# Kernel optimization log

Measured on AMD Instinct MI355X. Metric: run time of the kernel, lower is better.

The kernel has to match this reference:

```python
import jax, jax.numpy as jnp
import numpy as np

DIM = 1024
NUM_HEADS = 16
DIM_HEAD = 64
FEATURE_DIM = 64
INNER = NUM_HEADS * DIM_HEAD
EPS = 1e-6


def setup_inputs() -> dict:
    key = jax.random.key(0)
    ks = jax.random.split(key, 7)
    x = jax.random.normal(ks[0], (4, 8192, DIM), dtype=jnp.float32)
    s = 1.0 / np.sqrt(DIM)
    Wq = jax.random.normal(ks[1], (DIM, INNER), dtype=jnp.float32) * s
    Wk = jax.random.normal(ks[2], (DIM, INNER), dtype=jnp.float32) * s
    Wv = jax.random.normal(ks[3], (DIM, INNER), dtype=jnp.float32) * s
    proj = jax.random.normal(ks[4], (DIM_HEAD, FEATURE_DIM), dtype=jnp.float32) / np.sqrt(FEATURE_DIM)
    Wo = jax.random.normal(ks[5], (INNER, DIM), dtype=jnp.float32) * (1.0 / np.sqrt(INNER))
    bo = jnp.zeros((DIM,), dtype=jnp.float32)
    return {"x": x, "Wq": Wq, "Wk": Wk, "Wv": Wv, "proj": proj, "Wo": Wo, "bo": bo}


def _feature_map(t, proj):
    # t: [b, h, n, d] -> relu(t @ proj) + eps : [b, h, n, f]
    return jax.nn.relu(jnp.einsum('bhnd,df->bhnf', t, proj)) + EPS


def reference(x, Wq, Wk, Wv, proj, Wo, bo):
    b, n, _ = x.shape
    def split_heads(t):
        return t.reshape(b, n, NUM_HEADS, DIM_HEAD).transpose(0, 2, 1, 3)  # [b,h,n,d]
    q = split_heads(x @ Wq)
    k = split_heads(x @ Wk)
    v = split_heads(x @ Wv)
    qf = _feature_map(q, proj)  # [b,h,n,f]
    kf = _feature_map(k, proj)  # [b,h,n,f]
    kv = jnp.einsum('bhnf,bhnd->bhfd', kf, v)          # [b,h,f,d]
    k_sum = kf.sum(axis=-2)                             # [b,h,f]
    num = jnp.einsum('bhnf,bhfd->bhnd', qf, kv)         # [b,h,n,d]
    den = jnp.einsum('bhnf,bhf->bhn', qf, k_sum) + EPS  # [b,h,n]
    out = num / den[..., None]
    out = out.transpose(0, 2, 1, 3).reshape(b, n, INNER)
    return out @ Wo + bo
```

## Files before the change

### kernel.cpp

```cpp
#include <hip/hip_runtime.h>

typedef unsigned short u16;
typedef unsigned int u32;
typedef __attribute__((ext_vector_type(4))) float f32x4;
typedef __attribute__((ext_vector_type(4))) u16 u16x4;
typedef __attribute__((ext_vector_type(8))) u16 u16x8;
typedef __attribute__((ext_vector_type(8))) __bf16 bf16x8;

#define FLA_EPS 1e-6f

__device__ __forceinline__ u16 f2b(float f) {
  union { float f; u32 u; } v; v.f = f;
  u32 r = v.u + 0x7FFFu + ((v.u >> 16) & 1u);
  return (u16)(r >> 16);
}
__device__ __forceinline__ float b2f(u16 h) {
  union { u32 u; float f; } v; v.u = ((u32)h) << 16; return v.f;
}
__device__ __forceinline__ float bsum8(bf16x8 v) {
  union { bf16x8 b; u16x8 u; } x; x.b = v;
  float s = 0.f;
#pragma unroll
  for (int e = 0; e < 8; ++e) s += b2f(x.u[e]);
  return s;
}
__device__ __forceinline__ void g2l16(const void* g, void* l) {
  __builtin_amdgcn_global_load_lds((__attribute__((address_space(1))) void*)g,
                                   (__attribute__((address_space(3))) void*)l,
                                   16, 0, 0);
}

__global__ void __launch_bounds__(256) cast_f32_bf16(const float* __restrict__ in,
                                                     u16* __restrict__ out) {
  size_t i = (size_t)blockIdx.x * 256 + threadIdx.x;
  const f32x4* p = (const f32x4*)in + i * 2;
  f32x4 a = p[0], b = p[1];
  u16x8 r;
  r[0] = f2b(a[0]); r[1] = f2b(a[1]); r[2] = f2b(a[2]); r[3] = f2b(a[3]);
  r[4] = f2b(b[0]); r[5] = f2b(b[1]); r[6] = f2b(b[2]); r[7] = f2b(b[3]);
  ((u16x8*)out)[i] = r;
}

__global__ void __launch_bounds__(256) transpose_cast(const float* __restrict__ W,
                                                      u16* __restrict__ Wt, int dim) {
  __shared__ float tile[64][65];
  const int t = threadIdx.x;
  const int k0 = blockIdx.x * 64, n0 = blockIdx.y * 64;
  const int r = t >> 4, c4 = (t & 15) * 4;
#pragma unroll
  for (int i = 0; i < 4; ++i) {
    f32x4 vv = *(const f32x4*)(W + (size_t)(k0 + r + i * 16) * dim + n0 + c4);
    tile[r + i * 16][c4 + 0] = vv[0];
    tile[r + i * 16][c4 + 1] = vv[1];
    tile[r + i * 16][c4 + 2] = vv[2];
    tile[r + i * 16][c4 + 3] = vv[3];
  }
  __syncthreads();
#pragma unroll
  for (int i = 0; i < 4; ++i) {
    int nrow = r + i * 16;
    u16x4 o;
#pragma unroll
    for (int j = 0; j < 4; ++j) o[j] = f2b(tile[c4 + j][nrow]);
    *(u16x4*)(Wt + (size_t)(n0 + nrow) * dim + k0 + c4) = o;
  }
}

__global__ void __launch_bounds__(256) fold_w(const float* __restrict__ Wq,
                                              const float* __restrict__ Wk,
                                              const float* __restrict__ proj,
                                              u16* __restrict__ WqkvT) {
  __shared__ float Wt[64][65];
  __shared__ float P[64][64];
  const int t = threadIdx.x;
  const int kbase = blockIdx.x * 64, h = blockIdx.y, sel = blockIdx.z;
  const float* W = sel ? Wk : Wq;
  {
    int row = t >> 2, cb = (t & 3) * 16;
#pragma unroll
    for (int i = 0; i < 4; ++i) {
      f32x4 vv = *(const f32x4*)(W + (size_t)(kbase + row) * 1024 + h * 64 + cb + i * 4);
      Wt[row][cb + i * 4 + 0] = vv[0]; Wt[row][cb + i * 4 + 1] = vv[1];
      Wt[row][cb + i * 4 + 2] = vv[2]; Wt[row][cb + i * 4 + 3] = vv[3];
      f32x4 pp = *(const f32x4*)(proj + (size_t)row * 64 + cb + i * 4);
      P[row][cb + i * 4 + 0] = pp[0]; P[row][cb + i * 4 + 1] = pp[1];
      P[row][cb + i * 4 + 2] = pp[2]; P[row][cb + i * 4 + 3] = pp[3];
    }
  }
  __syncthreads();
  const int kk = t & 63, fg = (t >> 6) * 16;
  float acc[16] = {};
  for (int d = 0; d < 64; ++d) {
    float w = Wt[kk][d];
#pragma unroll
    for (int ff = 0; ff < 16; ++ff) acc[ff] = fmaf(w, P[d][fg + ff], acc[ff]);
  }
#pragma unroll
  for (int ff = 0; ff < 16; ++ff)
    WqkvT[(size_t)(sel * 1024 + h * 64 + fg + ff) * 1024 + kbase + kk] = f2b(acc[ff]);
}

template <int NB, bool QKV>
__global__ void __launch_bounds__(512) gemm256(const u16* __restrict__ Ax,
                                               const u16* __restrict__ Bt,
                                               u16* __restrict__ qo, u16* __restrict__ ko,
                                               u16* __restrict__ vo,
                                               float* __restrict__ Cf,
                                               const float* __restrict__ bias) {
  extern __shared__ __align__(16) u16 lds[];
  const int tid = threadIdx.x;
  const int flat = blockIdx.x;
  const int xcd = flat & 7, slot = flat >> 3;
  const int pos = slot & 7, g = slot >> 3;
  const int nc = g % NB, mc = g / NB;
  const int m0 = (xcd * 16 + mc * 8 + pos) * 256;
  const int n0 = nc * 256;
  const int w = tid >> 6, l = tid & 63, quad = l >> 4, lr = l & 15;
  const int wm = w >> 2, wn = w & 3;
  u16* const A0 = lds;
  u16* const B0 = lds + 16384;
  u16* const A1 = lds + 32768;
  u16* const B1 = lds + 49152;
  const int c0 = ((quad * 16) ^ ((lr & 7) << 4)) >> 1;
  const int c1 = ((64 + quad * 16) ^ ((lr & 7) << 4)) >> 1;
  const int rst = tid >> 3;
  const int ksw8 = ((tid & 7) ^ (rst & 7)) * 8;
  const int tid8 = tid * 8;

  f32x4 acc[8][4] = {};
  bf16x8 af[4][2];
  bf16x8 bl[2][2];
  bf16x8 bh[2][2];

#define STG(SRC, ROW0, KT, DST) do {                                         \
    const u16* s_ = (SRC) + (size_t)((ROW0) + rst) * 1024 + (KT) + ksw8;     \
    g2l16(s_, (DST) + tid8);                                                 \
    g2l16(s_ + 64 * 1024, (DST) + 4096 + tid8);                              \
  } while (0)

#define RD_A(BASE, MH) do {                                                  \
    const u16* ap_ = (BASE) + wm * 8192 + (MH) * 4096;                       \
    _Pragma("unroll")                                                        \
    for (int ii = 0; ii < 4; ++ii) {                                         \
      const int ro_ = (ii * 16 + lr) * 64;                                   \
      af[ii][0] = *(const bf16x8*)(ap_ + ro_ + c0);                          \
      af[ii][1] = *(const bf16x8*)(ap_ + ro_ + c1);                          \
    } } while (0)

#define RD_B(DST2, BASE, J0) do {                                            \
    const u16* bp_ = (BASE) + (wn >> 1) * 8192 + (wn & 1) * 4096;            \
    _Pragma("unroll")                                                        \
    for (int jj = 0; jj < 2; ++jj) {                                         \
      const int ro_ = (((J0) + jj) * 16 + lr) * 64;                          \
      DST2[jj][0] = *(const bf16x8*)(bp_ + ro_ + c0);                        \
      DST2[jj][1] = *(const bf16x8*)(bp_ + ro_ + c1);                        \
    } } while (0)

#define CL(MH, BF2, NH) do {                                                 \
    __builtin_amdgcn_s_setprio(1);                                           \
    _Pragma("unroll")                                                        \
    for (int ii = 0; ii < 4; ++ii)                                           \
      _Pragma("unroll")                                                      \
      for (int jj = 0; jj < 2; ++jj)                                         \
        _Pragma("unroll")                                                    \
        for (int ks = 0; ks < 2; ++ks)                                       \
          acc[(MH) * 4 + ii][(NH) * 2 + jj] =                                \
              __builtin_amdgcn_mfma_f32_16x16x32_bf16(                       \
                  af[ii][ks], BF2[jj][ks],                                   \
                  acc[(MH) * 4 + ii][(NH) * 2 + jj], 0, 0, 0);               \
    __builtin_amdgcn_s_setprio(0);                                           \
  } while (0)

#define SB0() __builtin_amdgcn_sched_barrier(0)
#define WAIT_LGKM(N) do { asm volatile("s_waitcnt lgkmcnt(" #N ")" ::: "memory"); SB0(); } while (0)
#define WAIT_VM0()   do { asm volatile("s_waitcnt vmcnt(0)" ::: "memory"); SB0(); } while (0)
#define BARRIER()    do { asm volatile("s_barrier" ::: "memory"); SB0(); } while (0)

  STG(Ax, m0, 0, A0); STG(Ax, m0 + 128, 0, A0 + 8192);
  STG(Bt, n0, 0, B0); STG(Bt, n0 + 128, 0, B0 + 8192);
  STG(Ax, m0, 64, A1); STG(Ax, m0 + 128, 64, A1 + 8192);
  STG(Bt, n0, 64, B1); STG(Bt, n0 + 128, 64, B1 + 8192);
  asm volatile("s_waitcnt vmcnt(8)" ::: "memory");
  SB0();
  BARRIER();
  RD_B(bl, B0, 0);
  RD_A(A0, 0);
  RD_B(bh, B0, 2);
  SB0();

#pragma unroll
  for (int t = 0; t < 16; ++t) {
    u16* const Ac = (t & 1) ? A1 : A0;
    u16* const Bc = (t & 1) ? B1 : B0;
    u16* const An = (t & 1) ? A0 : A1;
    u16* const Bn = (t & 1) ? B0 : B1;
    WAIT_LGKM(4);
    CL(0, bl, 0);
    WAIT_LGKM(0);
    CL(0, bh, 1);
    SB0();
    RD_A(Ac, 1);
    WAIT_LGKM(0);
    CL(1, bl, 0);
    SB0();
    if (t < 15) {
      WAIT_VM0();
      BARRIER();
      if (t < 14) {
        STG(Ax, m0,       (t + 2) * 64, Ac);
        STG(Ax, m0 + 128, (t + 2) * 64, Ac + 8192);
        STG(Bt, n0,       (t + 2) * 64, Bc);
        STG(Bt, n0 + 128, (t + 2) * 64, Bc + 8192);
      }
      RD_B(bl, Bn, 0);
      SB0();
    }
    CL(1, bh, 1);
    SB0();
    if (t < 15) {
      RD_A(An, 0);
      RD_B(bh, Bn, 2);
      SB0();
    }
  }
#undef STG
#undef RD_A
#undef RD_B
#undef CL
#undef WAIT_LGKM
#undef WAIT_VM0
#undef BARRIER

  const int rbase = m0 + wm * 128 + quad * 4;
  if (QKV) {
    const int sel = n0 >> 10;
    if (sel == 0) {
      const int cb = (n0 & 1023) + wn * 64 + lr;
#pragma unroll
      for (int mi = 0; mi < 8; ++mi)
#pragma unroll
        for (int nj = 0; nj < 4; ++nj)
#pragma unroll
          for (int rr = 0; rr < 4; ++rr) {
            int row = rbase + mi * 16 + rr;
            float v = fmaxf(acc[mi][nj][rr], 0.0f) + FLA_EPS;
            qo[(size_t)row * 1024 + cb + nj * 16] = f2b(v);
          }
    } else {
      const bool isK = (sel == 1);
      __syncthreads();
#pragma unroll
      for (int mi = 0; mi < 8; ++mi)
#pragma unroll
        for (int nj = 0; nj < 4; ++nj) {
          const int r0 = wm * 128 + mi * 16 + quad * 4;
          const int c = wn * 64 + nj * 16 + lr;
          u16x4 pk;
#pragma unroll
          for (int rr = 0; rr < 4; ++rr) {
            float v = acc[mi][nj][rr];
            if (isK) v = fmaxf(v, 0.0f) + FLA_EPS;
            pk[rr] = f2b(v);
          }
          *(u16x4*)&lds[c * 256 + (((r0 >> 3) ^ (c & 7)) << 3) + (r0 & 7)] = pk;
        }
      __syncthreads();
      u16* dstT = isK ? ko : vo;
      const int bI = m0 >> 13, s0 = m0 & 8191;
      const size_t cb0 = ((size_t)bI << 10) + (n0 & 1023);
#pragma unroll
      for (int i = 0; i < 16; ++i) {
        const int c = w * 32 + i * 2 + (l >> 5);
        const int u = (l & 31) ^ (c & 7);
        u16x8 vv = *(const u16x8*)&lds[c * 256 + u * 8];
        *(u16x8*)(dstT + (cb0 + c) * 8192 + s0 + (l & 31) * 8) = vv;
      }
    }
  } else {
#pragma unroll
    for (int mi = 0; mi < 8; ++mi)
#pragma unroll
      for (int nj = 0; nj < 4; ++nj) {
        const int cb = n0 + wn * 64 + nj * 16 + lr;
#pragma unroll
        for (int rr = 0; rr < 4; ++rr) {
          int row = rbase + mi * 16 + rr;
          Cf[(size_t)row * 1024 + cb] = acc[mi][nj][rr] + bias[cb];
        }
      }
  }
}

__global__ void __launch_bounds__(256) kv_mfma(const u16* __restrict__ kT,
                                               const u16* __restrict__ vT,
                                               float* __restrict__ part,
                                               float* __restrict__ ksum_p) {
  __shared__ __align__(16) u16 Av[2][4096];
  __shared__ __align__(16) u16 Bk[2][4096];
  const int tid = threadIdx.x;
  const int bh = blockIdx.x, chunk = blockIdx.y;
  const size_t n0 = (size_t)chunk * 1024;
  const u16* vbp = vT + (size_t)bh * 64 * 8192;
  const u16* kbp = kT + (size_t)bh * 64 * 8192;
  const int w = tid >> 6, l = tid & 63, quad = l >> 4, lr = l & 15;
  const int wd = w >> 1, wf = w & 1;
  const int dstg = tid >> 3, kc = tid & 7;
  const int sc0 = (kc ^ (dstg & 7)) * 8;
  f32x4 acc[2][2] = {};
  float ksm[2] = {0.f, 0.f};

#define KVSTG(BUF, T) do {                                                    \
    const size_t off_ = n0 + (size_t)(T) * 64;                                \
    g2l16(vbp + (size_t)dstg * 8192 + off_ + sc0, &Av[BUF][tid8_]);           \
    g2l16(vbp + (size_t)(dstg + 32) * 8192 + off_ + sc0, &Av[BUF][2048 + tid8_]); \
    g2l16(kbp + (size_t)dstg * 8192 + off_ + sc0, &Bk[BUF][tid8_]);           \
    g2l16(kbp + (size_t)(dstg + 32) * 8192 + off_ + sc0, &Bk[BUF][2048 + tid8_]); \
  } while (0)
  const int tid8_ = tid * 8;

  KVSTG(0, 0);
  for (int t = 0; t < 16; ++t) {
    const int buf = t & 1;
    if (t < 15) {
      KVSTG(buf ^ 1, t + 1);
      asm volatile("s_waitcnt vmcnt(4)" ::: "memory");
    } else {
      asm volatile("s_waitcnt vmcnt(0)" ::: "memory");
    }
    __builtin_amdgcn_sched_barrier(0);
    __builtin_amdgcn_s_barrier();
    bf16x8 av[2][2], bk[2][2];
#pragma unroll
    for (int di = 0; di < 2; ++di)
#pragma unroll
      for (int ks = 0; ks < 2; ++ks) {
        const int d = wd * 32 + di * 16 + lr;
        av[di][ks] = *(const bf16x8*)&Av[buf][d * 64 + ((ks * 4 + quad) ^ (d & 7)) * 8];
        const int f = wf * 32 + di * 16 + lr;
        bk[di][ks] = *(const bf16x8*)&Bk[buf][f * 64 + ((ks * 4 + quad) ^ (f & 7)) * 8];
      }
    asm volatile("s_waitcnt lgkmcnt(0)" ::: "memory");
    __builtin_amdgcn_sched_barrier(0);
#pragma unroll
    for (int di = 0; di < 2; ++di)
#pragma unroll
      for (int fj = 0; fj < 2; ++fj)
#pragma unroll
        for (int ks = 0; ks < 2; ++ks)
          acc[di][fj] = __builtin_amdgcn_mfma_f32_16x16x32_bf16(
              av[di][ks], bk[fj][ks], acc[di][fj], 0, 0, 0);
    if (w < 2) {
#pragma unroll
      for (int fj = 0; fj < 2; ++fj) {
        ksm[fj] += bsum8(bk[fj][0]);
        ksm[fj] += bsum8(bk[fj][1]);
      }
    }
    __builtin_amdgcn_s_barrier();
  }
#undef KVSTG

  float* pb = part + ((size_t)bh * 8 + chunk) * 4096;
#pragma unroll
  for (int di = 0; di < 2; ++di)
#pragma unroll
    for (int fj = 0; fj < 2; ++fj)
#pragma unroll
      for (int rr = 0; rr < 4; ++rr) {
        const int d = wd * 32 + di * 16 + quad * 4 + rr;
        const int f = wf * 32 + fj * 16 + lr;
        pb[d * 64 + f] = acc[di][fj][rr];
      }
  if (w < 2) {
#pragma unroll
    for (int fj = 0; fj < 2; ++fj) {
      float s = ksm[fj];
      s += __shfl_xor(s, 16, 64);
      s += __shfl_xor(s, 32, 64);
      if (l < 16)
        ksum_p[((size_t)bh * 8 + chunk) * 64 + wf * 32 + fj * 16 + l] = s;
    }
  }
}

__global__ void __launch_bounds__(256) reduce_kv(const float* __restrict__ part,
                                                 float* __restrict__ kvT) {
  int i = blockIdx.x * 256 + threadIdx.x;
  int bh = i >> 12, dfi = i & 4095;
  const float* p = part + (size_t)bh * 8 * 4096 + dfi;
  float s = 0.f;
#pragma unroll
  for (int sub = 0; sub < 8; ++sub) s += p[(size_t)sub * 4096];
  kvT[i] = s;
}

__global__ void __launch_bounds__(256) num_den(const u16* __restrict__ qf,
                                               const float* __restrict__ kvT,
                                               const float* __restrict__ ksum_p,
                                               u16* __restrict__ outI) {
  __shared__ __align__(16) u16 As[128 * 64];
  __shared__ __align__(16) u16 Bs[64 * 64];
  __shared__ float ksum_s[64];
  __shared__ float den_s[128];
  const int t = threadIdx.x;
  const size_t tok0 = (size_t)blockIdx.x * 128;
  const int h = blockIdx.y;
  const int bh = (blockIdx.x >> 6) * 16 + h;
  const int w = t >> 6, l = t & 63, quad = l >> 4, lr = l & 15;
  const int trow = t >> 3, tcol = (t & 7) * 8;
#pragma unroll
  for (int i = 0; i < 4; ++i) {
    int r = i * 32 + trow;
    g2l16(qf + (tok0 + r) * 1024 + h * 64 + tcol, &As[r * 64 + tcol]);
  }
  {
    const float* kvb = kvT + (size_t)bh * 4096;
    int d = t >> 2, cb = (t & 3) * 16;
    u16x8 o0, o1;
#pragma unroll
    for (int q4 = 0; q4 < 2; ++q4) {
      f32x4 vv = *(const f32x4*)(kvb + d * 64 + cb + q4 * 4);
      o0[q4 * 4 + 0] = f2b(vv[0]); o0[q4 * 4 + 1] = f2b(vv[1]);
      o0[q4 * 4 + 2] = f2b(vv[2]); o0[q4 * 4 + 3] = f2b(vv[3]);
    }
#pragma unroll
    for (int q4 = 0; q4 < 2; ++q4) {
      f32x4 vv = *(const f32x4*)(kvb + d * 64 + cb + 8 + q4 * 4);
      o1[q4 * 4 + 0] = f2b(vv[0]); o1[q4 * 4 + 1] = f2b(vv[1]);
      o1[q4 * 4 + 2] = f2b(vv[2]); o1[q4 * 4 + 3] = f2b(vv[3]);
    }
    *(u16x8*)&Bs[d * 64 + cb] = o0;
    *(u16x8*)&Bs[d * 64 + cb + 8] = o1;
  }
  if (t < 64) {
    float s = 0.f;
    const float* kp = ksum_p + (size_t)bh * 8 * 64 + t;
#pragma unroll
    for (int sub = 0; sub < 8; ++sub) s += kp[(size_t)sub * 64];
    ksum_s[t] = s;
  }
  __syncthreads();
  if (t < 128) {
    float d = FLA_EPS;
#pragma unroll
    for (int jj = 0; jj < 64; ++jj) {
      int f = (t + jj) & 63;
      d += b2f(As[t * 64 + f]) * ksum_s[f];
    }
    den_s[t] = d;
  }
  __syncthreads();
  f32x4 acc[2][4] = {};
  const int wrow = w * 32;
#pragma unroll
  for (int ks = 0; ks < 2; ++ks) {
    bf16x8 af[2], bfr[4];
#pragma unroll
    for (int i = 0; i < 2; ++i)
      af[i] = *(const bf16x8*)&As[(wrow + i * 16 + lr) * 64 + ks * 32 + quad * 8];
#pragma unroll
    for (int j = 0; j < 4; ++j)
      bfr[j] = *(const bf16x8*)&Bs[(j * 16 + lr) * 64 + ks * 32 + quad * 8];
#pragma unroll
    for (int i = 0; i < 2; ++i)
#pragma unroll
      for (int j = 0; j < 4; ++j)
        acc[i][j] = __builtin_amdgcn_mfma_f32_16x16x32_bf16(af[i], bfr[j], acc[i][j], 0, 0, 0);
  }
#pragma unroll
  for (int i = 0; i < 2; ++i)
#pragma unroll
    for (int j = 0; j < 4; ++j)
#pragma unroll
      for (int rr = 0; rr < 4; ++rr) {
        int rloc = wrow + i * 16 + quad * 4 + rr;
        float v = acc[i][j][rr] / den_s[rloc];
        outI[(tok0 + rloc) * 1024 + h * 64 + j * 16 + lr] = f2b(v);
      }
}

extern "C" void kernel_launch(void* const* d_in, const int* in_sizes, int n_in,
                              void* d_out, int out_size, void* d_ws, size_t ws_size,
                              hipStream_t stream) {
  const float* x    = (const float*)d_in[0];
  const float* Wq   = (const float*)d_in[1];
  const float* Wk   = (const float*)d_in[2];
  const float* Wv   = (const float*)d_in[3];
  const float* proj = (const float*)d_in[4];
  const float* Wo   = (const float*)d_in[5];
  const float* bo   = (const float*)d_in[6];
  float* out = (float*)d_out;

  char* ws = (char*)d_ws;
  const size_t SZ = 1ull << 26;
  u16* xb     = (u16*)(ws + 0);
  u16* qb     = (u16*)(ws + SZ);
  u16* kb     = (u16*)(ws + 2 * SZ);
  u16* vb     = (u16*)(ws + 3 * SZ);
  u16* WqkvT  = (u16*)(ws + 4 * SZ);
  u16* woT    = (u16*)(ws + 4 * SZ + 0x600000);
  float* part   = (float*)(ws + 4 * SZ + 0x800000);
  float* ksum_p = (float*)(ws + 4 * SZ + 0x800000 + 0x2000000);
  float* kvT    = (float*)(ws + 4 * SZ + 0x800000 + 0x2080000);

  static int attr_done = 0;
  if (!attr_done) {
    (void)hipFuncSetAttribute((const void*)gemm256<12, true>,
                              hipFuncAttributeMaxDynamicSharedMemorySize, 131072);
    (void)hipFuncSetAttribute((const void*)gemm256<4, false>,
                              hipFuncAttributeMaxDynamicSharedMemorySize, 131072);
    attr_done = 1;
  }

  cast_f32_bf16<<<16384, 256, 0, stream>>>(x, xb);
  fold_w<<<dim3(16, 16, 2), 256, 0, stream>>>(Wq, Wk, proj, WqkvT);
  transpose_cast<<<dim3(16, 16), 256, 0, stream>>>(Wv, WqkvT + (size_t)2048 * 1024, 1024);
  transpose_cast<<<dim3(16, 16), 256, 0, stream>>>(Wo, woT, 1024);
  gemm256<12, true><<<1536, 512, 131072, stream>>>(xb, WqkvT, qb, kb, vb, nullptr, nullptr);
  kv_mfma<<<dim3(64, 8), 256, 0, stream>>>(kb, vb, part, ksum_p);
  reduce_kv<<<1024, 256, 0, stream>>>(part, kvT);
  num_den<<<dim3(256, 16), 256, 0, stream>>>(qb, kvT, ksum_p, xb);
  gemm256<4, false><<<512, 512, 131072, stream>>>(xb, woT, nullptr, nullptr, nullptr, out, bo);
}
```

Measured before the change: 586.3 us.

## Merge prep kernels into one launch and reduce KV partials with atomics

The four preprocessing kernels (x cast, Wq/Wk fold with proj, Wv/Wo transpose-cast) become one launch that dispatches on block index. That launch also zeroes the kv and ksum accumulators. kv_mfma now atomically adds its per-chunk results straight into the final kvT and ksum buffers, which removes the reduce_kv kernel and the partial-sum buffers. This cuts launch overhead and partial-buffer traffic, at the cost of float atomics that make the summation order nondeterministic.

```diff
diff --git a/kernel.cpp b/kernel.cpp
--- a/kernel.cpp
+++ b/kernel.cpp
@@ -30,74 +30,88 @@
                                    16, 0, 0);
 }
 
-__global__ void __launch_bounds__(256) cast_f32_bf16(const float* __restrict__ in,
-                                                     u16* __restrict__ out) {
-  size_t i = (size_t)blockIdx.x * 256 + threadIdx.x;
-  const f32x4* p = (const f32x4*)in + i * 2;
-  f32x4 a = p[0], b = p[1];
-  u16x8 r;
-  r[0] = f2b(a[0]); r[1] = f2b(a[1]); r[2] = f2b(a[2]); r[3] = f2b(a[3]);
-  r[4] = f2b(b[0]); r[5] = f2b(b[1]); r[6] = f2b(b[2]); r[7] = f2b(b[3]);
-  ((u16x8*)out)[i] = r;
-}
-
-__global__ void __launch_bounds__(256) transpose_cast(const float* __restrict__ W,
-                                                      u16* __restrict__ Wt, int dim) {
-  __shared__ float tile[64][65];
+__global__ void __launch_bounds__(256) prep(const float* __restrict__ x,
+                                            const float* __restrict__ Wq,
+                                            const float* __restrict__ Wk,
+                                            const float* __restrict__ Wv,
+                                            const float* __restrict__ Wo,
+                                            const float* __restrict__ proj,
+                                            u16* __restrict__ xb,
+                                            u16* __restrict__ WqkvT,
+                                            u16* __restrict__ woT,
+                                            float* __restrict__ zbase) {
+  __shared__ __align__(16) char smem[33280];
+  const int blk = blockIdx.x;
   const int t = threadIdx.x;
-  const int k0 = blockIdx.x * 64, n0 = blockIdx.y * 64;
-  const int r = t >> 4, c4 = (t & 15) * 4;
-#pragma unroll
-  for (int i = 0; i < 4; ++i) {
-    f32x4 vv = *(const f32x4*)(W + (size_t)(k0 + r + i * 16) * dim + n0 + c4);
-    tile[r + i * 16][c4 + 0] = vv[0];
-    tile[r + i * 16][c4 + 1] = vv[1];
-    tile[r + i * 16][c4 + 2] = vv[2];
-    tile[r + i * 16][c4 + 3] = vv[3];
-  }
-  __syncthreads();
-#pragma unroll
-  for (int i = 0; i < 4; ++i) {
-    int nrow = r + i * 16;
-    u16x4 o;
-#pragma unroll
-    for (int j = 0; j < 4; ++j) o[j] = f2b(tile[c4 + j][nrow]);
-    *(u16x4*)(Wt + (size_t)(n0 + nrow) * dim + k0 + c4) = o;
-  }
-}
-
-__global__ void __launch_bounds__(256) fold_w(const float* __restrict__ Wq,
-                                              const float* __restrict__ Wk,
-                                              const float* __restrict__ proj,
-                                              u16* __restrict__ WqkvT) {
-  __shared__ float Wt[64][65];
-  __shared__ float P[64][64];
-  const int t = threadIdx.x;
-  const int kbase = blockIdx.x * 64, h = blockIdx.y, sel = blockIdx.z;
-  const float* W = sel ? Wk : Wq;
-  {
-    int row = t >> 2, cb = (t & 3) * 16;
+  if (blk < 16384) {
+    size_t i = (size_t)blk * 256 + t;
+    const f32x4* p = (const f32x4*)x + i * 2;
+    f32x4 a = p[0], b = p[1];
+    u16x8 r;
+    r[0] = f2b(a[0]); r[1] = f2b(a[1]); r[2] = f2b(a[2]); r[3] = f2b(a[3]);
+    r[4] = f2b(b[0]); r[5] = f2b(b[1]); r[6] = f2b(b[2]); r[7] = f2b(b[3]);
+    ((u16x8*)xb)[i] = r;
+  } else if (blk < 16896) {
+    const int b2 = blk - 16384;
+    const int kbase = (b2 & 15) * 64, h = (b2 >> 4) & 15, sel = b2 >> 8;
+    float (*Wt)[65] = (float(*)[65])smem;
+    float (*P)[64] = (float(*)[64])(smem + 16640);
+    const float* W = sel ? Wk : Wq;
+    {
+      int row = t >> 2, cb = (t & 3) * 16;
+#pragma unroll
+      for (int i = 0; i < 4; ++i) {
+        f32x4 vv = *(const f32x4*)(W + (size_t)(kbase + row) * 1024 + h * 64 + cb + i * 4);
+        Wt[row][cb + i * 4 + 0] = vv[0]; Wt[row][cb + i * 4 + 1] = vv[1];
+        Wt[row][cb + i * 4 + 2] = vv[2]; Wt[row][cb + i * 4 + 3] = vv[3];
+        f32x4 pp = *(const f32x4*)(proj + (size_t)row * 64 + cb + i * 4);
+        P[row][cb + i * 4 + 0] = pp[0]; P[row][cb + i * 4 + 1] = pp[1];
+        P[row][cb + i * 4 + 2] = pp[2]; P[row][cb + i * 4 + 3] = pp[3];
+      }
+    }
+    __syncthreads();
+    const int kk = t & 63, fg = (t >> 6) * 16;
+    float acc[16] = {};
+    for (int d = 0; d < 64; ++d) {
+      float w = Wt[kk][d];
+#pragma unroll
+      for (int ff = 0; ff < 16; ++ff) acc[ff] = fmaf(w, P[d][fg + ff], acc[ff]);
+    }
+#pragma unroll
+    for (int ff = 0; ff < 16; ++ff)
+      WqkvT[(size_t)(sel * 1024 + h * 64 + fg + ff) * 1024 + kbase + kk] = f2b(acc[ff]);
+  } else if (blk < 17408) {
+    const bool isV = blk < 17152;
+    const int b3 = blk - (isV ? 16896 : 17152);
+    const float* W = isV ? Wv : Wo;
+    u16* Wt_out = isV ? (WqkvT + (size_t)2048 * 1024) : woT;
+    float (*tile)[65] = (float(*)[65])smem;
+    const int k0 = (b3 & 15) * 64, n0 = (b3 >> 4) * 64;
+    const int r = t >> 4, c4 = (t & 15) * 4;
 #pragma unroll
     for (int i = 0; i < 4; ++i) {
-      f32x4 vv = *(const f32x4*)(W + (size_t)(kbase + row) * 1024 + h * 64 + cb + i * 4);
-      Wt[row][cb + i * 4 + 0] = vv[0]; Wt[row][cb + i * 4 + 1] = vv[1];
-      Wt[row][cb + i * 4 + 2] = vv[2]; Wt[row][cb + i * 4 + 3] = vv[3];
-      f32x4 pp = *(const f32x4*)(proj + (size_t)row * 64 + cb + i * 4);
-      P[row][cb + i * 4 + 0] = pp[0]; P[row][cb + i * 4 + 1] = pp[1];
-      P[row][cb + i * 4 + 2] = pp[2]; P[row][cb + i * 4 + 3] = pp[3];
-    }
-  }
-  __syncthreads();
-  const int kk = t & 63, fg = (t >> 6) * 16;
-  float acc[16] = {};
-  for (int d = 0; d < 64; ++d) {
-    float w = Wt[kk][d];
-#pragma unroll
-    for (int ff = 0; ff < 16; ++ff) acc[ff] = fmaf(w, P[d][fg + ff], acc[ff]);
-  }
-#pragma unroll
-  for (int ff = 0; ff < 16; ++ff)
-    WqkvT[(size_t)(sel * 1024 + h * 64 + fg + ff) * 1024 + kbase + kk] = f2b(acc[ff]);
+      f32x4 vv = *(const f32x4*)(W + (size_t)(k0 + r + i * 16) * 1024 + n0 + c4);
+      tile[r + i * 16][c4 + 0] = vv[0];
+      tile[r + i * 16][c4 + 1] = vv[1];
+      tile[r + i * 16][c4 + 2] = vv[2];
+      tile[r + i * 16][c4 + 3] = vv[3];
+    }
+    __syncthreads();
+#pragma unroll
+    for (int i = 0; i < 4; ++i) {
+      int nrow = r + i * 16;
+      u16x4 o;
+#pragma unroll
+      for (int j = 0; j < 4; ++j) o[j] = f2b(tile[c4 + j][nrow]);
+      *(u16x4*)(Wt_out + (size_t)(n0 + nrow) * 1024 + k0 + c4) = o;
+    }
+  } else {
+    const size_t i = (size_t)(blk - 17408) * 256 + t;
+    if (i < 66560) {
+      f32x4 z = {0.f, 0.f, 0.f, 0.f};
+      ((f32x4*)zbase)[i] = z;
+    }
+  }
 }
 
 template <int NB, bool QKV>
@@ -293,8 +307,8 @@
 
 __global__ void __launch_bounds__(256) kv_mfma(const u16* __restrict__ kT,
                                                const u16* __restrict__ vT,
-                                               float* __restrict__ part,
-                                               float* __restrict__ ksum_p) {
+                                               float* __restrict__ kvT,
+                                               float* __restrict__ ksum) {
   __shared__ __align__(16) u16 Av[2][4096];
   __shared__ __align__(16) u16 Bk[2][4096];
   const int tid = threadIdx.x;
@@ -360,7 +374,7 @@
   }
 #undef KVSTG
 
-  float* pb = part + ((size_t)bh * 8 + chunk) * 4096;
+  float* pb = kvT + (size_t)bh * 4096;
 #pragma unroll
   for (int di = 0; di < 2; ++di)
 #pragma unroll
@@ -369,7 +383,7 @@
       for (int rr = 0; rr < 4; ++rr) {
         const int d = wd * 32 + di * 16 + quad * 4 + rr;
         const int f = wf * 32 + fj * 16 + lr;
-        pb[d * 64 + f] = acc[di][fj][rr];
+        atomicAdd(&pb[d * 64 + f], acc[di][fj][rr]);
       }
   if (w < 2) {
 #pragma unroll
@@ -378,25 +392,14 @@
       s += __shfl_xor(s, 16, 64);
       s += __shfl_xor(s, 32, 64);
       if (l < 16)
-        ksum_p[((size_t)bh * 8 + chunk) * 64 + wf * 32 + fj * 16 + l] = s;
-    }
-  }
-}
-
-__global__ void __launch_bounds__(256) reduce_kv(const float* __restrict__ part,
-                                                 float* __restrict__ kvT) {
-  int i = blockIdx.x * 256 + threadIdx.x;
-  int bh = i >> 12, dfi = i & 4095;
-  const float* p = part + (size_t)bh * 8 * 4096 + dfi;
-  float s = 0.f;
-#pragma unroll
-  for (int sub = 0; sub < 8; ++sub) s += p[(size_t)sub * 4096];
-  kvT[i] = s;
+        atomicAdd(&ksum[(size_t)bh * 64 + wf * 32 + fj * 16 + l], s);
+    }
+  }
 }
 
 __global__ void __launch_bounds__(256) num_den(const u16* __restrict__ qf,
                                                const float* __restrict__ kvT,
-                                               const float* __restrict__ ksum_p,
+                                               const float* __restrict__ ksum,
                                                u16* __restrict__ outI) {
   __shared__ __align__(16) u16 As[128 * 64];
   __shared__ __align__(16) u16 Bs[64 * 64];
@@ -432,13 +435,7 @@
     *(u16x8*)&Bs[d * 64 + cb] = o0;
     *(u16x8*)&Bs[d * 64 + cb + 8] = o1;
   }
-  if (t < 64) {
-    float s = 0.f;
-    const float* kp = ksum_p + (size_t)bh * 8 * 64 + t;
-#pragma unroll
-    for (int sub = 0; sub < 8; ++sub) s += kp[(size_t)sub * 64];
-    ksum_s[t] = s;
-  }
+  if (t < 64) ksum_s[t] = ksum[(size_t)bh * 64 + t];
   __syncthreads();
   if (t < 128) {
     float d = FLA_EPS;
@@ -499,9 +496,8 @@
   u16* vb     = (u16*)(ws + 3 * SZ);
   u16* WqkvT  = (u16*)(ws + 4 * SZ);
   u16* woT    = (u16*)(ws + 4 * SZ + 0x600000);
-  float* part   = (float*)(ws + 4 * SZ + 0x800000);
-  float* ksum_p = (float*)(ws + 4 * SZ + 0x800000 + 0x2000000);
-  float* kvT    = (float*)(ws + 4 * SZ + 0x800000 + 0x2080000);
+  float* kvT    = (float*)(ws + 4 * SZ + 0x800000);
+  float* ksum   = (float*)(ws + 4 * SZ + 0x800000 + 0x100000);
 
   static int attr_done = 0;
   if (!attr_done) {
@@ -512,13 +508,9 @@
     attr_done = 1;
   }
 
-  cast_f32_bf16<<<16384, 256, 0, stream>>>(x, xb);
-  fold_w<<<dim3(16, 16, 2), 256, 0, stream>>>(Wq, Wk, proj, WqkvT);
-  transpose_cast<<<dim3(16, 16), 256, 0, stream>>>(Wv, WqkvT + (size_t)2048 * 1024, 1024);
-  transpose_cast<<<dim3(16, 16), 256, 0, stream>>>(Wo, woT, 1024);
+  prep<<<17668, 256, 0, stream>>>(x, Wq, Wk, Wv, Wo, proj, xb, WqkvT, woT, kvT);
   gemm256<12, true><<<1536, 512, 131072, stream>>>(xb, WqkvT, qb, kb, vb, nullptr, nullptr);
-  kv_mfma<<<dim3(64, 8), 256, 0, stream>>>(kb, vb, part, ksum_p);
-  reduce_kv<<<1024, 256, 0, stream>>>(part, kvT);
-  num_den<<<dim3(256, 16), 256, 0, stream>>>(qb, kvT, ksum_p, xb);
+  kv_mfma<<<dim3(64, 8), 256, 0, stream>>>(kb, vb, kvT, ksum);
+  num_den<<<dim3(256, 16), 256, 0, stream>>>(qb, kvT, ksum, xb);
   gemm256<4, false><<<512, 512, 131072, stream>>>(xb, woT, nullptr, nullptr, nullptr, out, bo);
 }
```

New measurement: 579.1 us. No clear change (-1.2%).
